# Performance work log

Hardware: AMD Instinct MI355X
Metric: run time of the kernel (lower is better)

The kernel has to match this reference:

```python
import jax, jax.numpy as jnp
import numpy as np

BOUND = 1.0 - 1e-16  # margin = 1e-16 (note: rounds to 1.0 in float32, same as torch float32)


def _lpc_to_par(a):
    # Backward Levinson-Durbin: LPC (K, a_1..a_M) -> PARCOR (K, k_1..k_M)
    K, c = a[..., :1], a[..., 1:]
    M = c.shape[-1]
    idx = jnp.arange(M)

    def step(c, m):  # m goes M, M-1, ..., 1
        k = jnp.take(c, m - 1, axis=-1)  # k_m = a_m^(m), shape (B,)
        # paired[j] = a_{m-1-j}^(m) for j=0..m-2 (i.e. a_{m-i} for i=1..m-1)
        paired = jnp.roll(jnp.flip(c, -1), -(M - m + 1), axis=-1)
        c2 = (c - k[..., None] * paired) / (1.0 - k[..., None] ** 2)
        c = jnp.where(idx < m - 1, c2, c)
        return c, k

    _, ks = jax.lax.scan(step, c, jnp.arange(M, 0, -1))
    k1 = jnp.flip(jnp.moveaxis(ks, 0, -1), -1)  # reorder to k_1..k_M, shape (B, M)
    return jnp.concatenate([K, k1], axis=-1)


def _par_to_lpc(k):
    # Forward Levinson-Durbin: PARCOR (K, k_1..k_M) -> LPC (K, a_1..a_M)
    K, kk = k[..., :1], k[..., 1:]
    M = kk.shape[-1]
    idx = jnp.arange(M)
    c0 = jnp.zeros_like(kk)

    def step(c, mk):  # m goes 1..M
        m, km = mk
        paired = jnp.roll(jnp.flip(c, -1), -(M - m + 1), axis=-1)
        c2 = c + km[..., None] * paired
        c = jnp.where(idx < m - 1, c2, c)
        c = jnp.where(idx == m - 1, km[..., None], c)
        return c, None

    ks = jnp.moveaxis(kk, -1, 0)  # (M, B)
    cM, _ = jax.lax.scan(step, c0, (jnp.arange(1, M + 1), ks))
    return jnp.concatenate([K, cM], axis=-1)


def setup_inputs() -> dict:
    key = jax.random.key(0)
    B, M = 2_000_000, 24
    # scale down so the backward Levinson recursion is well-conditioned
    a = 0.05 * jax.random.normal(key, (B, M + 1), dtype=jnp.float32)
    return {"a": a}


def reference(a):
    k = _lpc_to_par(a)
    K, k1 = k[..., :1], k[..., 1:]
    # warn_type='ignore': no side effect; just clip to stability bound
    k1 = jnp.clip(k1, -BOUND, BOUND)
    k2 = jnp.concatenate([K, k1], axis=-1)
    return _par_to_lpc(k2)
```

## Files before the change

### kernel.cpp

```cpp
#include <hip/hip_runtime.h>

#define MM 24
#define ROW_LEN (MM + 1)
#define RPB 64
#define FPB (RPB * ROW_LEN)
#define V4PB (FPB / 4)
#define NIT ((V4PB + RPB - 1) / RPB)

__global__ __launch_bounds__(RPB)
void lpc_stab_kernel(const float* __restrict__ a, float* __restrict__ out, int B) {
    __shared__ float lds[FPB];

    const long long total4 = ((long long)B * ROW_LEN) >> 2;
    const long long base4  = (long long)blockIdx.x * V4PB;
    const float4* a4 = (const float4*)a;
    float4*       o4 = (float4*)out;
    float4*       l4 = (float4*)lds;

    const bool interior = (base4 + V4PB) <= total4;

    if (interior) {
        #pragma unroll
        for (int it = 0; it < NIT; ++it) {
            int li = it * RPB + threadIdx.x;
            if (li < V4PB) l4[li] = a4[base4 + li];
        }
    } else {
        #pragma unroll
        for (int it = 0; it < NIT; ++it) {
            int li = it * RPB + threadIdx.x;
            if (li < V4PB && base4 + li < total4) l4[li] = a4[base4 + li];
        }
    }
    __syncthreads();

    const int row = blockIdx.x * RPB + threadIdx.x;
    if (row < B) {
        float* p = lds + threadIdx.x * ROW_LEN;
        float K = p[0];
        float c[MM], k[MM];
        #pragma unroll
        for (int j = 0; j < MM; ++j) c[j] = p[j + 1];

        #pragma unroll
        for (int m = MM; m >= 1; --m) {
            float km = c[m - 1];
            k[m - 1] = fminf(fmaxf(km, -1.0f), 1.0f);
            if (m >= 2) {
                float inv = __builtin_amdgcn_rcpf(1.0f - km * km);
                #pragma unroll
                for (int i = 0; i < (m - 1) / 2; ++i) {
                    float x = c[i], y = c[m - 2 - i];
                    c[i]         = (x - km * y) * inv;
                    c[m - 2 - i] = (y - km * x) * inv;
                }
                if ((m - 1) & 1) {
                    int i = (m - 1) / 2;
                    float x = c[i];
                    c[i] = (x - km * x) * inv;
                }
            }
        }

        #pragma unroll
        for (int m = 1; m <= MM; ++m) {
            float km = k[m - 1];
            #pragma unroll
            for (int i = 0; i < (m - 1) / 2; ++i) {
                float x = c[i], y = c[m - 2 - i];
                c[i]         = x + km * y;
                c[m - 2 - i] = y + km * x;
            }
            if ((m >= 2) && ((m - 1) & 1)) {
                int i = (m - 1) / 2;
                c[i] = c[i] + km * c[i];
            }
            c[m - 1] = km;
        }

        p[0] = K;
        #pragma unroll
        for (int j = 0; j < MM; ++j) p[j + 1] = c[j];
    }
    __syncthreads();

    if (interior) {
        #pragma unroll
        for (int it = 0; it < NIT; ++it) {
            int li = it * RPB + threadIdx.x;
            if (li < V4PB) o4[base4 + li] = l4[li];
        }
    } else {
        #pragma unroll
        for (int it = 0; it < NIT; ++it) {
            int li = it * RPB + threadIdx.x;
            if (li < V4PB && base4 + li < total4) o4[base4 + li] = l4[li];
        }
    }
}

extern "C" void kernel_launch(void* const* d_in, const int* in_sizes, int n_in,
                              void* d_out, int out_size, void* d_ws, size_t ws_size,
                              hipStream_t stream) {
    const float* a = (const float*)d_in[0];
    float* out = (float*)d_out;
    int B = in_sizes[0] / ROW_LEN;
    int blocks = (B + RPB - 1) / RPB;
    lpc_stab_kernel<<<blocks, RPB, 0, stream>>>(a, out, B);
}
```

Before: 334.4 us.

## Use persistent blocks with double-buffered async global-to-LDS tile staging

Replaces the one-tile-per-block kernel with a capped persistent grid that loops over tiles in a grid stride. The next tile is prefetched into a second LDS buffer with global_load_lds while the current tile is computed and stored, and vmcnt waits replace block-wide synchronisation for the loads. This is meant to hide global memory latency behind the Levinson recursion compute and to cut block launch overhead. It relies on hand-counted vmcnt values and single-wave blocks, so a miscount or a change in block size would break correctness, and the remainder rows are handled by a slow scalar path.

```diff
diff --git a/kernel.cpp b/kernel.cpp
--- a/kernel.cpp
+++ b/kernel.cpp
@@ -1,101 +1,144 @@
 #include <hip/hip_runtime.h>
 
 #define MM 24
-#define ROW_LEN (MM + 1)
+#define ROW_LEN 25
 #define RPB 64
-#define FPB (RPB * ROW_LEN)
-#define V4PB (FPB / 4)
-#define NIT ((V4PB + RPB - 1) / RPB)
+#define TILE_F (RPB * ROW_LEN)
+#define MAX_BLOCKS (256 * 12)
 
-__global__ __launch_bounds__(RPB)
-void lpc_stab_kernel(const float* __restrict__ a, float* __restrict__ out, int B) {
-    __shared__ float lds[FPB];
+__device__ __forceinline__ void gl_lds16(const float* g, float* l) {
+    __builtin_amdgcn_global_load_lds((const __attribute__((address_space(1))) void*)g,
+                                     (__attribute__((address_space(3))) void*)l,
+                                     16, 0, 0);
+}
+__device__ __forceinline__ void gl_lds4(const float* g, float* l) {
+    __builtin_amdgcn_global_load_lds((const __attribute__((address_space(1))) void*)g,
+                                     (__attribute__((address_space(3))) void*)l,
+                                     4, 0, 0);
+}
 
-    const long long total4 = ((long long)B * ROW_LEN) >> 2;
-    const long long base4  = (long long)blockIdx.x * V4PB;
-    const float4* a4 = (const float4*)a;
-    float4*       o4 = (float4*)out;
-    float4*       l4 = (float4*)lds;
+#define WAIT_VM(N) asm volatile("s_waitcnt vmcnt(" #N ")" ::: "memory")
 
-    const bool interior = (base4 + V4PB) <= total4;
+__device__ __forceinline__ void stage_tile(const float* __restrict__ a, float* buf,
+                                           long long tile, int lane) {
+    const float* g = a + tile * (long long)TILE_F;
+    #pragma unroll
+    for (int i = 0; i < 6; ++i)
+        gl_lds16(g + i * 256 + lane * 4, buf + i * 256);
+    gl_lds4(g + 1536 + lane, buf + 1536);
+}
 
-    if (interior) {
-        #pragma unroll
-        for (int it = 0; it < NIT; ++it) {
-            int li = it * RPB + threadIdx.x;
-            if (li < V4PB) l4[li] = a4[base4 + li];
-        }
-    } else {
-        #pragma unroll
-        for (int it = 0; it < NIT; ++it) {
-            int li = it * RPB + threadIdx.x;
-            if (li < V4PB && base4 + li < total4) l4[li] = a4[base4 + li];
-        }
-    }
-    __syncthreads();
+__device__ __forceinline__ void store_tile(float* __restrict__ outp, const float* buf,
+                                           long long tile, int lane) {
+    float4 r[6];
+    #pragma unroll
+    for (int i = 0; i < 6; ++i)
+        r[i] = *(const float4*)(buf + i * 256 + lane * 4);
+    float rt = buf[1536 + lane];
+    float* g = outp + tile * (long long)TILE_F;
+    #pragma unroll
+    for (int i = 0; i < 6; ++i)
+        *(float4*)(g + i * 256 + lane * 4) = r[i];
+    g[1536 + lane] = rt;
+}
 
-    const int row = blockIdx.x * RPB + threadIdx.x;
-    if (row < B) {
-        float* p = lds + threadIdx.x * ROW_LEN;
-        float K = p[0];
-        float c[MM], k[MM];
-        #pragma unroll
-        for (int j = 0; j < MM; ++j) c[j] = p[j + 1];
+__device__ __forceinline__ void lpc_row(float* p) {
+    float c[MM], k[MM];
+    #pragma unroll
+    for (int j = 0; j < MM; ++j) c[j] = p[j + 1];
 
-        #pragma unroll
-        for (int m = MM; m >= 1; --m) {
-            float km = c[m - 1];
-            k[m - 1] = fminf(fmaxf(km, -1.0f), 1.0f);
-            if (m >= 2) {
-                float inv = __builtin_amdgcn_rcpf(1.0f - km * km);
-                #pragma unroll
-                for (int i = 0; i < (m - 1) / 2; ++i) {
-                    float x = c[i], y = c[m - 2 - i];
-                    c[i]         = (x - km * y) * inv;
-                    c[m - 2 - i] = (y - km * x) * inv;
-                }
-                if ((m - 1) & 1) {
-                    int i = (m - 1) / 2;
-                    float x = c[i];
-                    c[i] = (x - km * x) * inv;
-                }
-            }
-        }
-
-        #pragma unroll
-        for (int m = 1; m <= MM; ++m) {
-            float km = k[m - 1];
+    #pragma unroll
+    for (int m = MM; m >= 1; --m) {
+        float km = c[m - 1];
+        k[m - 1] = fminf(fmaxf(km, -1.0f), 1.0f);
+        if (m >= 2) {
+            float inv = __builtin_amdgcn_rcpf(1.0f - km * km);
             #pragma unroll
             for (int i = 0; i < (m - 1) / 2; ++i) {
                 float x = c[i], y = c[m - 2 - i];
-                c[i]         = x + km * y;
-                c[m - 2 - i] = y + km * x;
+                c[i]         = (x - km * y) * inv;
+                c[m - 2 - i] = (y - km * x) * inv;
             }
-            if ((m >= 2) && ((m - 1) & 1)) {
+            if ((m - 1) & 1) {
                 int i = (m - 1) / 2;
-                c[i] = c[i] + km * c[i];
+                float x = c[i];
+                c[i] = (x - km * x) * inv;
             }
-            c[m - 1] = km;
         }
+    }
 
-        p[0] = K;
+    #pragma unroll
+    for (int m = 1; m <= MM; ++m) {
+        float km = k[m - 1];
         #pragma unroll
-        for (int j = 0; j < MM; ++j) p[j + 1] = c[j];
+        for (int i = 0; i < (m - 1) / 2; ++i) {
+            float x = c[i], y = c[m - 2 - i];
+            c[i]         = x + km * y;
+            c[m - 2 - i] = y + km * x;
+        }
+        if ((m >= 2) && ((m - 1) & 1)) {
+            int i = (m - 1) / 2;
+            c[i] = c[i] + km * c[i];
+        }
+        c[m - 1] = km;
     }
-    __syncthreads();
 
-    if (interior) {
+    #pragma unroll
+    for (int j = 0; j < MM; ++j) p[j + 1] = c[j];
+}
+
+__global__ __launch_bounds__(RPB, 3)
+void lpc_stab_kernel(const float* __restrict__ a, float* __restrict__ out,
+                     long long ntiles, int rem) {
+    __shared__ float bufA[TILE_F];
+    __shared__ float bufB[TILE_F];
+    const int lane = threadIdx.x;
+    const long long gstride = gridDim.x;
+    long long t = blockIdx.x;
+
+    if (t < ntiles) {
+        stage_tile(a, bufA, t, lane);
+        float* cur = bufA;
+        float* nxt = bufB;
+        long long t1 = t + gstride;
+        if (t1 < ntiles) {
+            stage_tile(a, bufB, t1, lane);
+            WAIT_VM(7);
+        } else {
+            WAIT_VM(0);
+        }
+        lpc_row(cur + lane * ROW_LEN);
+        __syncthreads();
+        store_tile(out, cur, t, lane);
+        t = t1;
+        { float* tmp = cur; cur = nxt; nxt = tmp; }
+
+        while (t < ntiles) {
+            const long long tn = t + gstride;
+            if (tn < ntiles) {
+                stage_tile(a, nxt, tn, lane);
+                WAIT_VM(14);
+            } else {
+                WAIT_VM(7);
+            }
+            lpc_row(cur + lane * ROW_LEN);
+            __syncthreads();
+            store_tile(out, cur, t, lane);
+            t = tn;
+            float* tmp = cur; cur = nxt; nxt = tmp;
+        }
+    }
+
+    if (rem && blockIdx.x == 0 && lane < rem) {
+        const long long r0 = ntiles * RPB + lane;
+        const float* gi = a + r0 * ROW_LEN;
+        float* p = bufA + lane * ROW_LEN;
         #pragma unroll
-        for (int it = 0; it < NIT; ++it) {
-            int li = it * RPB + threadIdx.x;
-            if (li < V4PB) o4[base4 + li] = l4[li];
-        }
-    } else {
+        for (int j = 0; j < ROW_LEN; ++j) p[j] = gi[j];
+        lpc_row(p);
+        float* go = out + r0 * ROW_LEN;
         #pragma unroll
-        for (int it = 0; it < NIT; ++it) {
-            int li = it * RPB + threadIdx.x;
-            if (li < V4PB && base4 + li < total4) o4[base4 + li] = l4[li];
-        }
+        for (int j = 0; j < ROW_LEN; ++j) go[j] = p[j];
     }
 }
 
@@ -104,7 +147,10 @@
                               hipStream_t stream) {
     const float* a = (const float*)d_in[0];
     float* out = (float*)d_out;
-    int B = in_sizes[0] / ROW_LEN;
-    int blocks = (B + RPB - 1) / RPB;
-    lpc_stab_kernel<<<blocks, RPB, 0, stream>>>(a, out, B);
+    long long B = (long long)in_sizes[0] / ROW_LEN;
+    long long ntiles = B / RPB;
+    int rem = (int)(B % RPB);
+    long long want = ntiles > 0 ? ntiles : 1;
+    int blocks = (int)(want < MAX_BLOCKS ? want : MAX_BLOCKS);
+    lpc_stab_kernel<<<blocks, RPB, 0, stream>>>(a, out, ntiles, rem);
 }
```

Measured after the change: 332.4 us. Within noise of the previous version (-0.6%).
